# Optimization experiments

Measured on AMD Instinct MI355X. Metric: run time of the kernel, lower is better.

## Reference

```python
import jax, jax.numpy as jnp
import numpy as np

D_MODEL = 1024
N_HEADS = 16
SEQ = 2048
BATCH = 2
EPS = 1e-5


def layer_norm(x, g, b):
    mu = jnp.mean(x, axis=-1, keepdims=True)
    var = jnp.mean(jnp.square(x - mu), axis=-1, keepdims=True)
    return (x - mu) * jax.lax.rsqrt(var + EPS) * g + b


def setup_inputs() -> dict:
    key = jax.random.key(0)
    ks = jax.random.split(key, 10)
    D = D_MODEL
    s = lambda fan_in: 1.0 / np.sqrt(fan_in)
    return {
        "x": jax.random.normal(ks[0], (BATCH, SEQ, D), dtype=jnp.float32),
        # weights stored [in, out] (torch Linear is y = x @ W.T; equivalent math)
        "w_attn": jax.random.uniform(ks[1], (D, 3 * D), minval=-s(D), maxval=s(D), dtype=jnp.float32),
        "b_attn": jnp.zeros((3 * D,), jnp.float32),
        "w_proj": jax.random.uniform(ks[2], (D, D), minval=-s(D), maxval=s(D), dtype=jnp.float32),
        "b_proj": jnp.zeros((D,), jnp.float32),
        "ln1_g": jnp.ones((D,), jnp.float32),
        "ln1_b": jnp.zeros((D,), jnp.float32),
        "ln2_g": jnp.ones((D,), jnp.float32),
        "ln2_b": jnp.zeros((D,), jnp.float32),
        "w_fc1": jax.random.uniform(ks[3], (D, 4 * D), minval=-s(D), maxval=s(D), dtype=jnp.float32),
        "b_fc1": jnp.zeros((4 * D,), jnp.float32),
        "w_fc2": jax.random.uniform(ks[4], (4 * D, D), minval=-s(4 * D), maxval=s(4 * D), dtype=jnp.float32),
        "b_fc2": jnp.zeros((D,), jnp.float32),
    }


def reference(x, w_attn, b_attn, w_proj, b_proj, ln1_g, ln1_b, ln2_g, ln2_b, w_fc1, b_fc1, w_fc2, b_fc2):
    B, L, D = x.shape
    H = N_HEADS
    Dh = D // H

    # --- attention sublayer ---
    h = layer_norm(x, ln1_g, ln1_b)
    qkv = h @ w_attn + b_attn                      # [B, L, 3D]
    # SOURCE BUG (faithful): q, k, v are all taken from the k third.
    k = qkv[..., D:2 * D]
    kh = k.reshape(B, L, H, Dh).transpose(0, 2, 1, 3)   # [B, H, L, Dh]
    att = jnp.einsum('bhqd,bhkd->bhqk', kh, kh) / jnp.sqrt(jnp.float32(Dh))
    att = jax.nn.softmax(att, axis=-1)
    out = jnp.einsum('bhqk,bhkd->bhqd', att, kh)         # [B, H, L, Dh]
    out = out.transpose(0, 2, 1, 3).reshape(B, L, D)
    x = x + (out @ w_proj + b_proj)

    # --- feed-forward sublayer ---
    h = layer_norm(x, ln2_g, ln2_b)
    h = jax.nn.relu(h @ w_fc1 + b_fc1)
    x = x + (h @ w_fc2 + b_fc2)
    return x
```

## Files before the change

kernel.cpp:

```cpp
#include <hip/hip_runtime.h>


typedef __attribute__((ext_vector_type(8))) short s8v;
typedef __attribute__((ext_vector_type(4))) short s4v;
typedef __attribute__((ext_vector_type(4))) float f4v;

#define D_MODEL 1024
#define SEQ 2048
#define BATCH 2
#define NH 16
#define DH 64
#define MROWS (BATCH * SEQ)

__device__ __forceinline__ float b2f(unsigned short u) {
  union { unsigned int i; float f; } v; v.i = ((unsigned int)u) << 16; return v.f;
}
__device__ __forceinline__ unsigned short f2b(float f) {
  unsigned int i = __builtin_bit_cast(unsigned int, f);
  unsigned int r = (i + 0x7fffu + ((i >> 16) & 1u)) >> 16;
  return (unsigned short)r;
}
__device__ __forceinline__ void async16(const void* g, void* l) {
  __builtin_amdgcn_global_load_lds(
      (const __attribute__((address_space(1))) unsigned int*)g,
      (__attribute__((address_space(3))) unsigned int*)l, 16, 0, 0);
}
__device__ __forceinline__ unsigned short cvt_b(float f) { return f2b(f); }
__device__ __forceinline__ unsigned short cvt_b(unsigned short u) { return u; }

#if __has_builtin(__builtin_amdgcn_mfma_f32_16x16x16_bf16)
__device__ __forceinline__ f4v mfma16(s4v a, s4v b, f4v c) {
  return __builtin_amdgcn_mfma_f32_16x16x16_bf16(a, b, c, 0, 0, 0);
}
#elif __has_builtin(__builtin_amdgcn_mfma_f32_16x16x16bf16_1k)
__device__ __forceinline__ f4v mfma16(s4v a, s4v b, f4v c) {
  return __builtin_amdgcn_mfma_f32_16x16x16bf16_1k(a, b, c, 0, 0, 0);
}
#else
__device__ __forceinline__ f4v mfma16(s4v a, s4v b, f4v c) {
  s8v aa = {a[0], a[1], a[2], a[3], 0, 0, 0, 0};
  s8v bb = {b[0], b[1], b[2], b[3], 0, 0, 0, 0};
  return __builtin_amdgcn_mfma_f32_16x16x32_bf16(aa, bb, c, 0, 0, 0);
}
#endif

__global__ __launch_bounds__(256) void ln_kernel(
    const float* __restrict__ x, const float* __restrict__ g,
    const float* __restrict__ bb, unsigned short* __restrict__ out) {
  int row = blockIdx.x;
  int t = threadIdx.x;
  const float* xr = x + (size_t)row * D_MODEL;
  float v[4];
  float s = 0.f, s2 = 0.f;
#pragma unroll
  for (int i = 0; i < 4; ++i) {
    float f = xr[t + 256 * i];
    v[i] = f; s += f; s2 += f * f;
  }
#pragma unroll
  for (int off = 1; off < 64; off <<= 1) {
    s += __shfl_xor(s, off, 64);
    s2 += __shfl_xor(s2, off, 64);
  }
  __shared__ float red[8];
  if ((t & 63) == 0) { red[t >> 6] = s; red[4 + (t >> 6)] = s2; }
  __syncthreads();
  s = red[0] + red[1] + red[2] + red[3];
  s2 = red[4] + red[5] + red[6] + red[7];
  float mu = s * (1.f / D_MODEL);
  float var = s2 * (1.f / D_MODEL) - mu * mu;
  float rstd = rsqrtf(var + 1e-5f);
#pragma unroll
  for (int i = 0; i < 4; ++i) {
    int c = t + 256 * i;
    float h = (v[i] - mu) * rstd * g[c] + bb[c];
    out[(size_t)row * D_MODEL + c] = f2b(h);
  }
}

template <typename T>
__global__ __launch_bounds__(256) void transpose_b(
    const T* __restrict__ src, unsigned short* __restrict__ dst,
    int srcStride, int dstStride, long long srcBatch, long long dstBatch) {
  __shared__ unsigned short tile[64][65];
  const T* s = src + (size_t)blockIdx.z * srcBatch;
  unsigned short* d = dst + (size_t)blockIdx.z * dstBatch;
  int n0 = blockIdx.x * 64, k0 = blockIdx.y * 64;
  for (int i = threadIdx.x; i < 4096; i += 256) {
    int k = i >> 6, n = i & 63;
    tile[k][n] = cvt_b(s[(size_t)(k0 + k) * srcStride + n0 + n]);
  }
  __syncthreads();
  for (int i = threadIdx.x; i < 4096; i += 256) {
    int n = i >> 6, k = i & 63;
    d[(size_t)(n0 + n) * dstStride + k0 + k] = tile[k][n];
  }
}

template <int RES, bool RELU, bool KH, int OUTF, int BN>
__global__ __launch_bounds__(256) void gemm_bt(
    const unsigned short* __restrict__ A, const unsigned short* __restrict__ Bt,
    const float* __restrict__ bias, const float* __restrict__ res,
    void* __restrict__ out, int M, int N, int K) {
  constexpr int NT = BN / 32;
  __shared__ __align__(16) unsigned short lsA[128 * 64];
  __shared__ __align__(16) unsigned short lsB[BN * 64];
  int tid = threadIdx.x;
  int lane = tid & 63, w = tid >> 6, quad = lane >> 4, l16 = lane & 15;
  int m0 = blockIdx.y * 128, n0 = blockIdx.x * BN;
  int wm = (w >> 1) * 64, wn = (w & 1) * (BN / 2);
  f4v acc[4][NT] = {};
  for (int kt = 0; kt < K; kt += 64) {
#pragma unroll
    for (int i = 0; i < 4; ++i) {
      int cb = w * 256 + i * 64;
      int ci = cb + lane;
      int row = ci >> 3, c = ci & 7;
      int cs = c ^ (row & 7);
      async16(A + (size_t)(m0 + row) * K + kt + cs * 8, &lsA[cb * 8]);
    }
#pragma unroll
    for (int i = 0; i < BN / 32; ++i) {
      int cb = w * (BN * 2) + i * 64;
      int ci = cb + lane;
      int row = ci >> 3, c = ci & 7;
      int cs = c ^ (row & 7);
      async16(Bt + (size_t)(n0 + row) * K + kt + cs * 8, &lsB[cb * 8]);
    }
    __builtin_amdgcn_s_waitcnt(0x0f70);
    __syncthreads();
#pragma unroll
    for (int s = 0; s < 2; ++s) {
      s8v af[4], bf[NT];
#pragma unroll
      for (int t = 0; t < 4; ++t) {
        int am = wm + t * 16 + l16;
        int ac = (s * 4 + quad) ^ (am & 7);
        af[t] = *(const s8v*)(&lsA[am * 64 + ac * 8]);
      }
#pragma unroll
      for (int t = 0; t < NT; ++t) {
        int bn = wn + t * 16 + l16;
        int bc = (s * 4 + quad) ^ (bn & 7);
        bf[t] = *(const s8v*)(&lsB[bn * 64 + bc * 8]);
      }
#pragma unroll
      for (int ti = 0; ti < 4; ++ti)
#pragma unroll
        for (int tj = 0; tj < NT; ++tj)
          acc[ti][tj] = __builtin_amdgcn_mfma_f32_16x16x32_bf16(
              af[ti], bf[tj], acc[ti][tj], 0, 0, 0);
    }
    __syncthreads();
  }
#pragma unroll
  for (int tj = 0; tj < NT; ++tj) {
    int col = n0 + wn + tj * 16 + l16;
    float bv = bias[col];
#pragma unroll
    for (int ti = 0; ti < 4; ++ti) {
#pragma unroll
      for (int r = 0; r < 4; ++r) {
        int rowg = m0 + wm + ti * 16 + quad * 4 + r;
        float vv = acc[ti][tj][r] + bv;
        if (RES == 2) vv += res[(size_t)rowg * N + col];
        if (RELU) vv = fmaxf(vv, 0.f);
        size_t oidx;
        if (KH) {
          int b = rowg >> 11, l = rowg & 2047, h = col >> 6, d = col & 63;
          oidx = (((size_t)(b * NH + h)) * SEQ + l) * DH + d;
        } else {
          oidx = (size_t)rowg * N + col;
        }
        if (OUTF == 0) ((unsigned short*)out)[oidx] = f2b(vv);
        else           ((float*)out)[oidx] = vv;
      }
    }
  }
}

__global__ __launch_bounds__(256) void flash_k(
    const unsigned short* __restrict__ kh, const unsigned short* __restrict__ khT,
    unsigned short* __restrict__ Opart, float* __restrict__ lpart) {
  __shared__ __align__(16) unsigned short lsK[128 * 64];
  __shared__ __align__(16) unsigned short lsKT[64 * 128];
  int tid = threadIdx.x;
  int lane = tid & 63, w = tid >> 6, quad = lane >> 4, l16 = lane & 15;
  int split = blockIdx.x, bh = blockIdx.y, qb = blockIdx.z;
  const unsigned short* khB = kh + (size_t)bh * SEQ * DH;
  const unsigned short* khTB = khT + (size_t)bh * DH * SEQ;
  unsigned short* Op = Opart + (size_t)split * MROWS * D_MODEL;
  float* lp = lpart + (size_t)split * BATCH * NH * SEQ;
  s8v aQ[2][2];
#pragma unroll
  for (int g = 0; g < 2; ++g) {
    int q = qb * 128 + w * 32 + g * 16 + l16;
#pragma unroll
    for (int s = 0; s < 2; ++s)
      aQ[g][s] = *(const s8v*)(khB + (size_t)q * DH + s * 32 + quad * 8);
  }
  float l_lane[2] = {0.f, 0.f};
  f4v accO[2][4] = {};
  const float kexp = 0.18033688f;

  for (int kt8 = 0; kt8 < 8; ++kt8) {
    int key0 = split * 1024 + kt8 * 128;
#pragma unroll
    for (int i = 0; i < 4; ++i) {
      int cb = w * 256 + i * 64;
      int ci = cb + lane;
      int row = ci >> 3, c = ci & 7;
      int cs = c ^ (row & 7);
      async16(khB + (size_t)(key0 + row) * DH + cs * 8, &lsK[cb * 8]);
    }
#pragma unroll
    for (int i = 0; i < 4; ++i) {
      int cb = w * 256 + i * 64;
      int ci = cb + lane;
      int row = ci >> 4, c = ci & 15;
      int cs = c ^ (row & 15);
      async16(khTB + (size_t)row * SEQ + key0 + cs * 8, &lsKT[cb * 8]);
    }
    __builtin_amdgcn_s_waitcnt(0x0f70);
    __syncthreads();
#pragma unroll
    for (int half = 0; half < 2; ++half) {
      f4v accST[2][4] = {};
#pragma unroll
      for (int s = 0; s < 2; ++s) {
#pragma unroll
        for (int tj = 0; tj < 4; ++tj) {
          int key = half * 64 + tj * 16 + l16;
          int c = (s * 4 + quad) ^ (key & 7);
          s8v kf = *(const s8v*)(&lsK[key * 64 + c * 8]);
#pragma unroll
          for (int g = 0; g < 2; ++g)
            accST[g][tj] = __builtin_amdgcn_mfma_f32_16x16x32_bf16(
                kf, aQ[g][s], accST[g][tj], 0, 0, 0);
        }
      }
#pragma unroll
      for (int tj = 0; tj < 4; ++tj) {
        s4v pf[2];
#pragma unroll
        for (int g = 0; g < 2; ++g) {
#pragma unroll
          for (int r = 0; r < 4; ++r) {
            float p = exp2f(accST[g][tj][r] * kexp);
            l_lane[g] += p;
            unsigned int pb = __builtin_bit_cast(unsigned int, p * 1.00195312f);
            pf[g][r] = (short)(pb >> 16);
          }
        }
#pragma unroll
        for (int db = 0; db < 4; ++db) {
          int d = db * 16 + l16;
          int ch = (half * 8 + tj * 2 + (quad >> 1)) ^ (d & 15);
          s4v vf = *(const s4v*)(&lsKT[d * 128 + ch * 8 + (quad & 1) * 4]);
#pragma unroll
          for (int g = 0; g < 2; ++g)
            accO[g][db] = mfma16(pf[g], vf, accO[g][db]);
        }
      }
    }
    __syncthreads();
  }
  int b = bh >> 4, h = bh & 15;
#pragma unroll
  for (int g = 0; g < 2; ++g) {
    float lv = l_lane[g];
    lv += __shfl_xor(lv, 16, 64);
    lv += __shfl_xor(lv, 32, 64);
    if (quad == 0) {
      int q = qb * 128 + w * 32 + g * 16 + l16;
      lp[(size_t)bh * SEQ + q] = lv;
    }
#pragma unroll
    for (int r = 0; r < 4; ++r) {
      int l = qb * 128 + w * 32 + g * 16 + quad * 4 + r;
#pragma unroll
      for (int db = 0; db < 4; ++db) {
        int d = db * 16 + l16;
        Op[((size_t)(b * SEQ + l)) * D_MODEL + h * DH + d] = f2b(accO[g][db][r]);
      }
    }
  }
}

__global__ __launch_bounds__(256) void attn_combine(
    const unsigned short* __restrict__ Opart, const float* __restrict__ lpart,
    unsigned short* __restrict__ attn) {
  int row = blockIdx.x;
  int b = row >> 11, l = row & 2047;
  int c0 = threadIdx.x * 4;
  int h = c0 >> 6;
  size_t lidx = (size_t)(b * NH + h) * SEQ + l;
  float ls = lpart[lidx] + lpart[(size_t)BATCH * NH * SEQ + lidx];
  float inv = 1.f / ls;
  s4v o0 = *(const s4v*)(Opart + (size_t)row * D_MODEL + c0);
  s4v o1 = *(const s4v*)(Opart + (size_t)MROWS * D_MODEL +
                         (size_t)row * D_MODEL + c0);
  s4v ov;
#pragma unroll
  for (int i = 0; i < 4; ++i)
    ov[i] = (short)f2b((b2f((unsigned short)o0[i]) +
                        b2f((unsigned short)o1[i])) * inv);
  *(s4v*)(attn + (size_t)row * D_MODEL + c0) = ov;
}

extern "C" void kernel_launch(void* const* d_in, const int* in_sizes, int n_in,
                              void* d_out, int out_size, void* d_ws, size_t ws_size,
                              hipStream_t stream) {
  (void)in_sizes; (void)n_in; (void)out_size;
  const float* x      = (const float*)d_in[0];
  const float* w_attn = (const float*)d_in[1];
  const float* b_attn = (const float*)d_in[2];
  const float* w_proj = (const float*)d_in[3];
  const float* b_proj = (const float*)d_in[4];
  const float* ln1_g  = (const float*)d_in[5];
  const float* ln1_b  = (const float*)d_in[6];
  const float* ln2_g  = (const float*)d_in[7];
  const float* ln2_b  = (const float*)d_in[8];
  const float* w_fc1  = (const float*)d_in[9];
  const float* b_fc1  = (const float*)d_in[10];
  const float* w_fc2  = (const float*)d_in[11];
  const float* b_fc2  = (const float*)d_in[12];

  char* ws = (char*)d_ws;
  float*          x1    = (float*)(ws);
  unsigned short* hbuf  = (unsigned short*)(ws + (size_t)(16u << 20));
  unsigned short* wT1   = (unsigned short*)(ws + (size_t)(24u << 20));
  unsigned short* wT2   = (unsigned short*)(ws + (size_t)(32u << 20));
  unsigned short* kh    = (unsigned short*)(ws + (size_t)(40u << 20));
  unsigned short* khT   = (unsigned short*)(ws + (size_t)(48u << 20));
  unsigned short* Opart = (unsigned short*)(ws);
  float*          lpart = (float*)(ws + (size_t)(16u << 20));
  unsigned short* fc1o  = kh;
  unsigned short* attn  = (unsigned short*)d_out;
  float* outf = (float*)d_out;
  bool big_ws = ws_size >= ((size_t)72u << 20);

  dim3 blk(256);
  hipLaunchKernelGGL(ln_kernel, dim3(MROWS), blk, 0, stream, x, ln1_g, ln1_b, hbuf);
  hipLaunchKernelGGL(transpose_b<float>, dim3(16, 16, 1), blk, 0, stream,
                     w_attn + 1024, wT1, 3 * D_MODEL, D_MODEL, 0LL, 0LL);
  hipLaunchKernelGGL((gemm_bt<0, false, true, 0, 64>), dim3(16, 32), blk, 0, stream,
                     hbuf, wT1, b_attn + 1024, nullptr, (void*)kh,
                     MROWS, D_MODEL, D_MODEL);
  hipLaunchKernelGGL(transpose_b<unsigned short>, dim3(1, 32, 32), blk, 0, stream,
                     kh, khT, DH, SEQ, (long long)(SEQ * DH), (long long)(DH * SEQ));
  hipLaunchKernelGGL(flash_k, dim3(2, 32, SEQ / 128), blk, 0, stream,
                     kh, khT, Opart, lpart);
  hipLaunchKernelGGL(attn_combine, dim3(MROWS), blk, 0, stream,
                     Opart, lpart, attn);
  hipLaunchKernelGGL(transpose_b<float>, dim3(16, 16, 1), blk, 0, stream,
                     w_proj, wT1, D_MODEL, D_MODEL, 0LL, 0LL);
  hipLaunchKernelGGL((gemm_bt<2, false, false, 1, 64>), dim3(16, 32), blk, 0, stream,
                     attn, wT1, b_proj, x, (void*)x1, MROWS, D_MODEL, D_MODEL);
  hipLaunchKernelGGL(ln_kernel, dim3(MROWS), blk, 0, stream, x1, ln2_g, ln2_b, hbuf);
  hipLaunchKernelGGL(transpose_b<float>, dim3(64, 16, 1), blk, 0, stream,
                     w_fc1, wT1, 4 * D_MODEL, D_MODEL, 0LL, 0LL);
  hipLaunchKernelGGL(transpose_b<float>, dim3(16, 64, 1), blk, 0, stream,
                     w_fc2, wT2, D_MODEL, 4 * D_MODEL, 0LL, 0LL);
  if (big_ws) {
    hipLaunchKernelGGL((gemm_bt<0, true, false, 0, 128>), dim3(32, 32), blk, 0, stream,
                       hbuf, wT1, b_fc1, nullptr, (void*)fc1o,
                       MROWS, 4 * D_MODEL, D_MODEL);
    hipLaunchKernelGGL((gemm_bt<2, false, false, 1, 64>), dim3(16, 32), blk, 0, stream,
                       fc1o, wT2, b_fc2, x1, (void*)outf,
                       MROWS, D_MODEL, 4 * D_MODEL);
  } else {
    for (int c = 0; c < 2; ++c) {
      const unsigned short* h2c = hbuf + (size_t)c * 2048 * D_MODEL;
      const float* x1c = x1 + (size_t)c * 2048 * D_MODEL;
      float* outc = outf + (size_t)c * 2048 * D_MODEL;
      hipLaunchKernelGGL((gemm_bt<0, true, false, 0, 128>), dim3(32, 16), blk, 0, stream,
                         h2c, wT1, b_fc1, nullptr, (void*)fc1o,
                         2048, 4 * D_MODEL, D_MODEL);
      hipLaunchKernelGGL((gemm_bt<2, false, false, 1, 64>), dim3(16, 16), blk, 0, stream,
                         fc1o, wT2, b_fc2, x1c, (void*)outc,
                         2048, D_MODEL, 4 * D_MODEL);
    }
  }
}
```

Before: 370.7 us.

## Fuse attention combine into proj GEMM and split-K the fc2 GEMM

Removes the attn_combine kernel by merging the two flash-attention partial outputs and normalizing them inside the A-tile load of a dedicated projection GEMM. Flash attention is launched twice, once per key split, so the partial buffers can alias freed workspace regions. The fc2 GEMM on the big-workspace path is split along K into two BN=128 launches, and a float4 epilogue kernel adds the residual and bias. This trades the extra combine pass for synchronous A loads that include a divide, and adds a separate fp32 partial-sum buffer plus an extra elementwise pass.

```diff
diff --git a/kernel.cpp b/kernel.cpp
--- a/kernel.cpp
+++ b/kernel.cpp
@@ -97,11 +97,11 @@
   }
 }
 
-template <int RES, bool RELU, bool KH, int OUTF, int BN>
+template <int RES, bool RELU, bool KH, int OUTF, int BN, bool HASB>
 __global__ __launch_bounds__(256) void gemm_bt(
     const unsigned short* __restrict__ A, const unsigned short* __restrict__ Bt,
     const float* __restrict__ bias, const float* __restrict__ res,
-    void* __restrict__ out, int M, int N, int K) {
+    void* __restrict__ out, int M, int N, int K, int lda, int ldb) {
   constexpr int NT = BN / 32;
   __shared__ __align__(16) unsigned short lsA[128 * 64];
   __shared__ __align__(16) unsigned short lsB[BN * 64];
@@ -117,7 +117,7 @@
       int ci = cb + lane;
       int row = ci >> 3, c = ci & 7;
       int cs = c ^ (row & 7);
-      async16(A + (size_t)(m0 + row) * K + kt + cs * 8, &lsA[cb * 8]);
+      async16(A + (size_t)(m0 + row) * lda + kt + cs * 8, &lsA[cb * 8]);
     }
 #pragma unroll
     for (int i = 0; i < BN / 32; ++i) {
@@ -125,7 +125,7 @@
       int ci = cb + lane;
       int row = ci >> 3, c = ci & 7;
       int cs = c ^ (row & 7);
-      async16(Bt + (size_t)(n0 + row) * K + kt + cs * 8, &lsB[cb * 8]);
+      async16(Bt + (size_t)(n0 + row) * ldb + kt + cs * 8, &lsB[cb * 8]);
     }
     __builtin_amdgcn_s_waitcnt(0x0f70);
     __syncthreads();
@@ -156,7 +156,7 @@
 #pragma unroll
   for (int tj = 0; tj < NT; ++tj) {
     int col = n0 + wn + tj * 16 + l16;
-    float bv = bias[col];
+    float bv = HASB ? bias[col] : 0.f;
 #pragma unroll
     for (int ti = 0; ti < 4; ++ti) {
 #pragma unroll
@@ -179,18 +179,102 @@
   }
 }
 
+__global__ __launch_bounds__(256) void gemm_proj(
+    const unsigned short* __restrict__ Op0, const unsigned short* __restrict__ Op1,
+    const float* __restrict__ lp0, const float* __restrict__ lp1,
+    const unsigned short* __restrict__ Bt, const float* __restrict__ bias,
+    const float* __restrict__ res, float* __restrict__ out) {
+  constexpr int N = D_MODEL, K = D_MODEL;
+  __shared__ __align__(16) unsigned short lsA[128 * 64];
+  __shared__ __align__(16) unsigned short lsB[64 * 64];
+  int tid = threadIdx.x;
+  int lane = tid & 63, w = tid >> 6, quad = lane >> 4, l16 = lane & 15;
+  int m0 = blockIdx.y * 128, n0 = blockIdx.x * 64;
+  int wm = (w >> 1) * 64, wn = (w & 1) * 32;
+  f4v acc[4][2] = {};
+  for (int kt = 0; kt < K; kt += 64) {
+    int h = kt >> 6;
+#pragma unroll
+    for (int i = 0; i < 4; ++i) {
+      int ci = tid + i * 256;
+      int row = ci >> 3, c = ci & 7;
+      int cs = c ^ (row & 7);
+      int rowg = m0 + row;
+      int bh = (rowg >> 11) * NH + h;
+      int l = rowg & 2047;
+      size_t lidx = (size_t)bh * SEQ + l;
+      float inv = 1.f / (lp0[lidx] + lp1[lidx]);
+      const unsigned short* a0 = Op0 + (size_t)rowg * D_MODEL + kt + cs * 8;
+      const unsigned short* a1 = Op1 + (size_t)rowg * D_MODEL + kt + cs * 8;
+      s8v v0 = *(const s8v*)a0;
+      s8v v1 = *(const s8v*)a1;
+      s8v av;
+#pragma unroll
+      for (int j = 0; j < 8; ++j)
+        av[j] = (short)f2b((b2f((unsigned short)v0[j]) +
+                            b2f((unsigned short)v1[j])) * inv);
+      *(s8v*)(&lsA[ci * 8]) = av;
+    }
+#pragma unroll
+    for (int i = 0; i < 2; ++i) {
+      int cb = w * 128 + i * 64;
+      int ci = cb + lane;
+      int row = ci >> 3, c = ci & 7;
+      int cs = c ^ (row & 7);
+      async16(Bt + (size_t)(n0 + row) * K + kt + cs * 8, &lsB[cb * 8]);
+    }
+    __builtin_amdgcn_s_waitcnt(0x0f70);
+    __syncthreads();
+#pragma unroll
+    for (int s = 0; s < 2; ++s) {
+      s8v af[4], bf[2];
+#pragma unroll
+      for (int t = 0; t < 4; ++t) {
+        int am = wm + t * 16 + l16;
+        int ac = (s * 4 + quad) ^ (am & 7);
+        af[t] = *(const s8v*)(&lsA[am * 64 + ac * 8]);
+      }
+#pragma unroll
+      for (int t = 0; t < 2; ++t) {
+        int bn = wn + t * 16 + l16;
+        int bc = (s * 4 + quad) ^ (bn & 7);
+        bf[t] = *(const s8v*)(&lsB[bn * 64 + bc * 8]);
+      }
+#pragma unroll
+      for (int ti = 0; ti < 4; ++ti)
+#pragma unroll
+        for (int tj = 0; tj < 2; ++tj)
+          acc[ti][tj] = __builtin_amdgcn_mfma_f32_16x16x32_bf16(
+              af[ti], bf[tj], acc[ti][tj], 0, 0, 0);
+    }
+    __syncthreads();
+  }
+#pragma unroll
+  for (int tj = 0; tj < 2; ++tj) {
+    int col = n0 + wn + tj * 16 + l16;
+    float bv = bias[col];
+#pragma unroll
+    for (int ti = 0; ti < 4; ++ti) {
+#pragma unroll
+      for (int r = 0; r < 4; ++r) {
+        int rowg = m0 + wm + ti * 16 + quad * 4 + r;
+        out[(size_t)rowg * N + col] =
+            acc[ti][tj][r] + bv + res[(size_t)rowg * N + col];
+      }
+    }
+  }
+}
+
 __global__ __launch_bounds__(256) void flash_k(
     const unsigned short* __restrict__ kh, const unsigned short* __restrict__ khT,
-    unsigned short* __restrict__ Opart, float* __restrict__ lpart) {
+    unsigned short* __restrict__ Op, float* __restrict__ lp, int split) {
   __shared__ __align__(16) unsigned short lsK[128 * 64];
   __shared__ __align__(16) unsigned short lsKT[64 * 128];
   int tid = threadIdx.x;
   int lane = tid & 63, w = tid >> 6, quad = lane >> 4, l16 = lane & 15;
-  int split = blockIdx.x, bh = blockIdx.y, qb = blockIdx.z;
+  int bh = blockIdx.x, qb = blockIdx.y;
   const unsigned short* khB = kh + (size_t)bh * SEQ * DH;
   const unsigned short* khTB = khT + (size_t)bh * DH * SEQ;
-  unsigned short* Op = Opart + (size_t)split * MROWS * D_MODEL;
-  float* lp = lpart + (size_t)split * BATCH * NH * SEQ;
   s8v aQ[2][2];
 #pragma unroll
   for (int g = 0; g < 2; ++g) {
@@ -287,25 +371,20 @@
   }
 }
 
-__global__ __launch_bounds__(256) void attn_combine(
-    const unsigned short* __restrict__ Opart, const float* __restrict__ lpart,
-    unsigned short* __restrict__ attn) {
-  int row = blockIdx.x;
-  int b = row >> 11, l = row & 2047;
-  int c0 = threadIdx.x * 4;
-  int h = c0 >> 6;
-  size_t lidx = (size_t)(b * NH + h) * SEQ + l;
-  float ls = lpart[lidx] + lpart[(size_t)BATCH * NH * SEQ + lidx];
-  float inv = 1.f / ls;
-  s4v o0 = *(const s4v*)(Opart + (size_t)row * D_MODEL + c0);
-  s4v o1 = *(const s4v*)(Opart + (size_t)MROWS * D_MODEL +
-                         (size_t)row * D_MODEL + c0);
-  s4v ov;
-#pragma unroll
-  for (int i = 0; i < 4; ++i)
-    ov[i] = (short)f2b((b2f((unsigned short)o0[i]) +
-                        b2f((unsigned short)o1[i])) * inv);
-  *(s4v*)(attn + (size_t)row * D_MODEL + c0) = ov;
+__global__ __launch_bounds__(256) void fuse_out(
+    const float* __restrict__ x1, const float* __restrict__ S0,
+    float* __restrict__ dout, const float* __restrict__ b2) {
+  size_t base = (size_t)blockIdx.x * 1024 + threadIdx.x * 4;
+  int c0 = (int)(base & 1023);
+  float4 a = *(const float4*)(x1 + base);
+  float4 b = *(const float4*)(S0 + base);
+  float4 c = *(const float4*)(dout + base);
+  float4 o;
+  o.x = a.x + b.x + c.x + b2[c0];
+  o.y = a.y + b.y + c.y + b2[c0 + 1];
+  o.z = a.z + b.z + c.z + b2[c0 + 2];
+  o.w = a.w + b.w + c.w + b2[c0 + 3];
+  *(float4*)(dout + base) = o;
 }
 
 extern "C" void kernel_launch(void* const* d_in, const int* in_sizes, int n_in,
@@ -327,16 +406,19 @@
   const float* b_fc2  = (const float*)d_in[12];
 
   char* ws = (char*)d_ws;
-  float*          x1    = (float*)(ws);
-  unsigned short* hbuf  = (unsigned short*)(ws + (size_t)(16u << 20));
-  unsigned short* wT1   = (unsigned short*)(ws + (size_t)(24u << 20));
-  unsigned short* wT2   = (unsigned short*)(ws + (size_t)(32u << 20));
-  unsigned short* kh    = (unsigned short*)(ws + (size_t)(40u << 20));
-  unsigned short* khT   = (unsigned short*)(ws + (size_t)(48u << 20));
-  unsigned short* Opart = (unsigned short*)(ws);
-  float*          lpart = (float*)(ws + (size_t)(16u << 20));
-  unsigned short* fc1o  = kh;
-  unsigned short* attn  = (unsigned short*)d_out;
+  float*          x1   = (float*)(ws);
+  unsigned short* hbuf = (unsigned short*)(ws + (size_t)(16u << 20));
+  unsigned short* wT1  = (unsigned short*)(ws + (size_t)(24u << 20));
+  unsigned short* wT2  = (unsigned short*)(ws + (size_t)(32u << 20));
+  unsigned short* kh   = (unsigned short*)(ws + (size_t)(40u << 20));
+  unsigned short* khT  = (unsigned short*)(ws + (size_t)(48u << 20));
+  unsigned short* Op0  = hbuf;
+  unsigned short* Op1  = wT1;
+  float*          lp0  = (float*)(ws + (size_t)(32u << 20));
+  float*          lp1  = lp0 + (size_t)BATCH * NH * SEQ;
+  unsigned short* wTp  = kh;
+  unsigned short* fc1o = kh;
+  float*          S0   = (float*)hbuf;
   float* outf = (float*)d_out;
   bool big_ws = ws_size >= ((size_t)72u << 20);
 
@@ -344,42 +426,47 @@
   hipLaunchKernelGGL(ln_kernel, dim3(MROWS), blk, 0, stream, x, ln1_g, ln1_b, hbuf);
   hipLaunchKernelGGL(transpose_b<float>, dim3(16, 16, 1), blk, 0, stream,
                      w_attn + 1024, wT1, 3 * D_MODEL, D_MODEL, 0LL, 0LL);
-  hipLaunchKernelGGL((gemm_bt<0, false, true, 0, 64>), dim3(16, 32), blk, 0, stream,
-                     hbuf, wT1, b_attn + 1024, nullptr, (void*)kh,
-                     MROWS, D_MODEL, D_MODEL);
+  hipLaunchKernelGGL((gemm_bt<0, false, true, 0, 64, true>), dim3(16, 32), blk, 0,
+                     stream, hbuf, wT1, b_attn + 1024, nullptr, (void*)kh,
+                     MROWS, D_MODEL, D_MODEL, D_MODEL, D_MODEL);
   hipLaunchKernelGGL(transpose_b<unsigned short>, dim3(1, 32, 32), blk, 0, stream,
                      kh, khT, DH, SEQ, (long long)(SEQ * DH), (long long)(DH * SEQ));
-  hipLaunchKernelGGL(flash_k, dim3(2, 32, SEQ / 128), blk, 0, stream,
-                     kh, khT, Opart, lpart);
-  hipLaunchKernelGGL(attn_combine, dim3(MROWS), blk, 0, stream,
-                     Opart, lpart, attn);
+  hipLaunchKernelGGL(flash_k, dim3(32, SEQ / 128), blk, 0, stream,
+                     kh, khT, Op0, lp0, 0);
+  hipLaunchKernelGGL(flash_k, dim3(32, SEQ / 128), blk, 0, stream,
+                     kh, khT, Op1, lp1, 1);
   hipLaunchKernelGGL(transpose_b<float>, dim3(16, 16, 1), blk, 0, stream,
-                     w_proj, wT1, D_MODEL, D_MODEL, 0LL, 0LL);
-  hipLaunchKernelGGL((gemm_bt<2, false, false, 1, 64>), dim3(16, 32), blk, 0, stream,
-                     attn, wT1, b_proj, x, (void*)x1, MROWS, D_MODEL, D_MODEL);
+                     w_proj, wTp, D_MODEL, D_MODEL, 0LL, 0LL);
+  hipLaunchKernelGGL(gemm_proj, dim3(16, 32), blk, 0, stream,
+                     Op0, Op1, lp0, lp1, wTp, b_proj, x, x1);
   hipLaunchKernelGGL(ln_kernel, dim3(MROWS), blk, 0, stream, x1, ln2_g, ln2_b, hbuf);
   hipLaunchKernelGGL(transpose_b<float>, dim3(64, 16, 1), blk, 0, stream,
                      w_fc1, wT1, 4 * D_MODEL, D_MODEL, 0LL, 0LL);
   hipLaunchKernelGGL(transpose_b<float>, dim3(16, 64, 1), blk, 0, stream,
                      w_fc2, wT2, D_MODEL, 4 * D_MODEL, 0LL, 0LL);
   if (big_ws) {
-    hipLaunchKernelGGL((gemm_bt<0, true, false, 0, 128>), dim3(32, 32), blk, 0, stream,
-                       hbuf, wT1, b_fc1, nullptr, (void*)fc1o,
-                       MROWS, 4 * D_MODEL, D_MODEL);
-    hipLaunchKernelGGL((gemm_bt<2, false, false, 1, 64>), dim3(16, 32), blk, 0, stream,
-                       fc1o, wT2, b_fc2, x1, (void*)outf,
-                       MROWS, D_MODEL, 4 * D_MODEL);
+    hipLaunchKernelGGL((gemm_bt<0, true, false, 0, 128, true>), dim3(32, 32), blk, 0,
+                       stream, hbuf, wT1, b_fc1, nullptr, (void*)fc1o,
+                       MROWS, 4 * D_MODEL, D_MODEL, D_MODEL, D_MODEL);
+    hipLaunchKernelGGL((gemm_bt<0, false, false, 1, 128, false>), dim3(8, 32), blk, 0,
+                       stream, fc1o, wT2, nullptr, nullptr, (void*)S0,
+                       MROWS, D_MODEL, 2 * D_MODEL, 4 * D_MODEL, 4 * D_MODEL);
+    hipLaunchKernelGGL((gemm_bt<0, false, false, 1, 128, false>), dim3(8, 32), blk, 0,
+                       stream, fc1o + 2 * D_MODEL, wT2 + 2 * D_MODEL, nullptr,
+                       nullptr, (void*)outf,
+                       MROWS, D_MODEL, 2 * D_MODEL, 4 * D_MODEL, 4 * D_MODEL);
+    hipLaunchKernelGGL(fuse_out, dim3(MROWS), blk, 0, stream, x1, S0, outf, b_fc2);
   } else {
     for (int c = 0; c < 2; ++c) {
       const unsigned short* h2c = hbuf + (size_t)c * 2048 * D_MODEL;
       const float* x1c = x1 + (size_t)c * 2048 * D_MODEL;
       float* outc = outf + (size_t)c * 2048 * D_MODEL;
-      hipLaunchKernelGGL((gemm_bt<0, true, false, 0, 128>), dim3(32, 16), blk, 0, stream,
-                         h2c, wT1, b_fc1, nullptr, (void*)fc1o,
-                         2048, 4 * D_MODEL, D_MODEL);
-      hipLaunchKernelGGL((gemm_bt<2, false, false, 1, 64>), dim3(16, 16), blk, 0, stream,
-                         fc1o, wT2, b_fc2, x1c, (void*)outc,
-                         2048, D_MODEL, 4 * D_MODEL);
-    }
-  }
-}
+      hipLaunchKernelGGL((gemm_bt<0, true, false, 0, 128, true>), dim3(32, 16), blk,
+                         0, stream, h2c, wT1, b_fc1, nullptr, (void*)fc1o,
+                         2048, 4 * D_MODEL, D_MODEL, D_MODEL, D_MODEL);
+      hipLaunchKernelGGL((gemm_bt<2, false, false, 1, 64, true>), dim3(16, 16), blk,
+                         0, stream, fc1o, wT2, b_fc2, x1c, (void*)outc,
+                         2048, D_MODEL, 4 * D_MODEL, 4 * D_MODEL, 4 * D_MODEL);
+    }
+  }
+}
```

After: 451.0 us. +21.6%, slower.
